# Kernel optimization log

Measured on AMD Instinct MI355X. Metric: run time of the kernel, lower is better.

Reference implementation:

```python
import jax, jax.numpy as jnp
import numpy as np
from jax import lax

NUM_LAYERS = 4
EPS_BN = 1e-5
EPS_AGG = 1e-6


def _bn(x, gamma, beta):
    # training-mode batch norm over the leading (node/edge) dim
    m = x.mean(axis=0)
    v = x.var(axis=0)
    return gamma * (x - m) / jnp.sqrt(v + EPS_BN) + beta


def setup_inputs() -> dict:
    key = jax.random.key(0)
    ks = jax.random.split(key, 32)
    N, E, D, L, K = 50000, 400000, 64, 128, 16
    s = 0.05
    inp = {
        'reads': jax.random.uniform(ks[0], (N, 4, L), jnp.float32),
        'src': jax.random.randint(ks[1], (E,), 0, N, jnp.int32),
        'dst': jax.random.randint(ks[2], (E,), 0, N, jnp.int32),
        'overlap_similarity': jax.random.uniform(ks[3], (E,), jnp.float32),
        'overlap_length': jax.random.normal(ks[4], (E,), jnp.float32),
        # sequence encoder conv: Conv1d(4 -> D, kernel K)
        'conv_w': jax.random.normal(ks[5], (D, 4, K), jnp.float32) * s,
        'conv_b': jnp.zeros((D,), jnp.float32),
        # edge encoder: Linear(2 -> D)
        'We': jax.random.normal(ks[6], (2, D), jnp.float32) * s,
        'be': jnp.zeros((D,), jnp.float32),
        # GatedGCN per-layer weights, stacked on leading layer dim
        'A1': jax.random.normal(ks[7], (NUM_LAYERS, D, D), jnp.float32) * s,
        'A2': jax.random.normal(ks[8], (NUM_LAYERS, D, D), jnp.float32) * s,
        'A3': jax.random.normal(ks[9], (NUM_LAYERS, D, D), jnp.float32) * s,
        'bA1': jnp.zeros((NUM_LAYERS, D), jnp.float32),
        'bA2': jnp.zeros((NUM_LAYERS, D), jnp.float32),
        'bA3': jnp.zeros((NUM_LAYERS, D), jnp.float32),
        'U': jax.random.normal(ks[10], (NUM_LAYERS, D, D), jnp.float32) * s,
        'V': jax.random.normal(ks[11], (NUM_LAYERS, D, D), jnp.float32) * s,
        'bU': jnp.zeros((NUM_LAYERS, D), jnp.float32),
        'bV': jnp.zeros((NUM_LAYERS, D), jnp.float32),
        'bn_h_gamma': jnp.ones((NUM_LAYERS, D), jnp.float32),
        'bn_h_beta': jnp.zeros((NUM_LAYERS, D), jnp.float32),
        'bn_e_gamma': jnp.ones((NUM_LAYERS, D), jnp.float32),
        'bn_e_beta': jnp.zeros((NUM_LAYERS, D), jnp.float32),
        # edge decoder MLP: Linear(3D -> D) -> ReLU -> Linear(D -> 1)
        'W1': jax.random.normal(ks[12], (3 * D, D), jnp.float32) * s,
        'b1': jnp.zeros((D,), jnp.float32),
        'W2': jax.random.normal(ks[13], (D, 1), jnp.float32) * s,
        'b2': jnp.zeros((1,), jnp.float32),
    }
    return inp


def reference(reads, src, dst, overlap_similarity, overlap_length,
              conv_w, conv_b, We, be,
              A1, A2, A3, bA1, bA2, bA3, U, V, bU, bV,
              bn_h_gamma, bn_h_beta, bn_e_gamma, bn_e_beta,
              W1, b1, W2, b2):
    N = reads.shape[0]
    # --- SequenceEncoder: Conv1d over one-hot reads, global max-pool ---
    hseq = lax.conv_general_dilated(
        reads, conv_w, window_strides=(1,), padding='VALID',
        dimension_numbers=('NCH', 'OIH', 'NCH'))  # [N, D, L-K+1]
    h = (hseq + conv_b[None, :, None]).max(axis=2)  # [N, D]
    # --- EdgeEncoder: Linear on [similarity, length] ---
    e = jnp.stack([overlap_similarity, overlap_length], axis=1) @ We + be  # [E, D]
    # --- stacked GatedGCN layers (gather src/dst, scatter-aggregate to dst) ---
    for l in range(NUM_LAYERS):
        hs = h[src]  # [E, D] gather
        hd = h[dst]
        e_hat = (hs @ A1[l] + bA1[l]) + (hd @ A2[l] + bA2[l]) + (e @ A3[l] + bA3[l])
        sigma = jax.nn.sigmoid(e_hat)  # edge gates
        Vh = hs @ V[l] + bV[l]
        num = jax.ops.segment_sum(sigma * Vh, dst, num_segments=N)  # [N, D]
        den = jax.ops.segment_sum(sigma, dst, num_segments=N)
        h_hat = (h @ U[l] + bU[l]) + num / (den + EPS_AGG)
        h = h + jax.nn.relu(_bn(h_hat, bn_h_gamma[l], bn_h_beta[l]))
        e = e + jax.nn.relu(_bn(e_hat, bn_e_gamma[l], bn_e_beta[l]))
    # --- EdgeDecoder: MLP on [h_src, h_dst, e] ---
    z = jnp.concatenate([h[src], h[dst], e], axis=1)  # [E, 3D]
    p = jax.nn.relu(z @ W1 + b1) @ W2 + b2  # [E, 1]
    return p
```

## Files before the change

kernel.cpp:

```cpp
#include <hip/hip_runtime.h>
#include <hip/hip_bf16.h>
#include <cstdint>
#include <cstddef>

#define DD 64

typedef __attribute__((ext_vector_type(8))) short short8;
typedef __attribute__((ext_vector_type(4))) float f32x4;

__device__ __forceinline__ float4 f4_0() { return make_float4(0.f, 0.f, 0.f, 0.f); }

__device__ __forceinline__ unsigned short f2bf(float f) {
  __hip_bfloat16 h = __float2bfloat16(f);
  return *reinterpret_cast<unsigned short*>(&h);
}
__device__ __forceinline__ float bfl(unsigned u) { return __uint_as_float(u << 16); }
__device__ __forceinline__ float bfh(unsigned u) { return __uint_as_float(u & 0xffff0000u); }
__device__ __forceinline__ float b2f(unsigned short u) {
  return __uint_as_float(((unsigned)u) << 16);
}

__device__ __forceinline__ short8 pack_bf16x8(float4 a, float4 b) {
  union { unsigned short us[8]; short8 v; } pk;
  pk.us[0] = f2bf(a.x); pk.us[1] = f2bf(a.y); pk.us[2] = f2bf(a.z); pk.us[3] = f2bf(a.w);
  pk.us[4] = f2bf(b.x); pk.us[5] = f2bf(b.y); pk.us[6] = f2bf(b.z); pk.us[7] = f2bf(b.w);
  return pk.v;
}

__device__ __forceinline__ short8 lds_frag(const unsigned short* p) {
  uint2 lo = *reinterpret_cast<const uint2*>(p);
  uint2 hi = *reinterpret_cast<const uint2*>(p + 4);
  union { unsigned u[4]; short8 v; } t;
  t.u[0] = lo.x; t.u[1] = lo.y; t.u[2] = hi.x; t.u[3] = hi.y;
  return t.v;
}
__device__ __forceinline__ short8 g_frag(const unsigned short* p) {
  return *reinterpret_cast<const short8*>(p);
}

__global__ __launch_bounds__(256) void k_hist(const int* __restrict__ dst,
                                              int* __restrict__ cnt, int E) {
  int j = blockIdx.x * 256 + threadIdx.x;
  if (j < E) atomicAdd(&cnt[dst[j]], 1);
}

__global__ __launch_bounds__(1024) void k_scan(const int* __restrict__ cnt,
                                               int* __restrict__ row_ptr,
                                               int* __restrict__ nxt, int N, int E) {
  __shared__ int wsum[16];
  __shared__ int carry_s;
  const int tid = threadIdx.x;
  const int wid = tid >> 6, lane = tid & 63;
  if (tid == 0) carry_s = 0;
  __syncthreads();
  const int ntl = (N + 4095) / 4096;
  for (int b = 0; b < ntl; ++b) {
    const int i0 = b * 4096 + tid * 4;
    int v0 = 0, v1 = 0, v2 = 0, v3 = 0;
    if (i0 + 3 < N) {
      int4 q = *reinterpret_cast<const int4*>(cnt + i0);
      v0 = q.x; v1 = q.y; v2 = q.z; v3 = q.w;
    } else {
      if (i0 < N) v0 = cnt[i0];
      if (i0 + 1 < N) v1 = cnt[i0 + 1];
      if (i0 + 2 < N) v2 = cnt[i0 + 2];
      if (i0 + 3 < N) v3 = cnt[i0 + 3];
    }
    const int tsum = v0 + v1 + v2 + v3;
    int x = tsum;
#pragma unroll
    for (int off = 1; off < 64; off <<= 1) {
      int y = __shfl_up(x, off, 64);
      if (lane >= off) x += y;
    }
    if (lane == 63) wsum[wid] = x;
    __syncthreads();
    if (wid == 0 && lane < 16) {
      int wv = wsum[lane];
#pragma unroll
      for (int off = 1; off < 16; off <<= 1) {
        int y = __shfl_up(wv, off, 64);
        if (lane >= off) wv += y;
      }
      wsum[lane] = wv;
    }
    __syncthreads();
    int base = carry_s + (wid > 0 ? wsum[wid - 1] : 0) + (x - tsum);
    int e1 = base + v0, e2 = e1 + v1, e3 = e2 + v2;
    if (i0 < N) { row_ptr[i0] = base; nxt[i0] = base; }
    if (i0 + 1 < N) { row_ptr[i0 + 1] = e1; nxt[i0 + 1] = e1; }
    if (i0 + 2 < N) { row_ptr[i0 + 2] = e2; nxt[i0 + 2] = e2; }
    if (i0 + 3 < N) { row_ptr[i0 + 3] = e3; nxt[i0 + 3] = e3; }
    __syncthreads();
    if (tid == 0) carry_s += wsum[15];
    __syncthreads();
  }
  if (tid == 0) row_ptr[N] = E;
}

__global__ __launch_bounds__(256) void k_scatter(const int* __restrict__ dst,
                                                 const int* __restrict__ src,
                                                 int* __restrict__ nxt,
                                                 int* __restrict__ order,
                                                 int* __restrict__ psrc,
                                                 int* __restrict__ pdst, int E) {
  int j = blockIdx.x * 256 + threadIdx.x;
  if (j >= E) return;
  int d = dst[j];
  int pos = atomicAdd(&nxt[d], 1);
  order[pos] = j;
  psrc[pos] = src[j];
  pdst[pos] = d;
}

__global__ __launch_bounds__(256) void k_prep(const float* __restrict__ A1,
                                              const float* __restrict__ A2,
                                              const float* __restrict__ V,
                                              const float* __restrict__ U,
                                              const float* __restrict__ A3,
                                              const float* __restrict__ W1,
                                              unsigned short* __restrict__ T) {
  const int b = blockIdx.x;
  const int tid = threadIdx.x;
  if (b < 20) {
    const int l = b / 5, m = b % 5;
    const float* srcp =
        (m == 0 ? A1 : m == 1 ? A2 : m == 2 ? V : m == 3 ? U : A3) + l * 4096;
    unsigned short* dstp = T + b * 4096;
    for (int i = tid; i < 4096; i += 256) {
      int n = i >> 6, k = i & 63;
      dstp[i] = f2bf(srcp[k * 64 + n]);
    }
  } else {
    unsigned short* dstp = T + 20 * 4096;
    for (int i = tid; i < 12288; i += 256) {
      int n = i / 192, k = i % 192;
      dstp[i] = f2bf(W1[k * 64 + n]);
    }
  }
}

__global__ __launch_bounds__(256) void k_conv_mfma(const float* __restrict__ reads,
                                                   const float* __restrict__ w,
                                                   const float* __restrict__ bias,
                                                   float* __restrict__ h, int N) {
  __shared__ unsigned short cp[4 * 4 * 4 * 144];
  const int tid = threadIdx.x;
  const int nb = blockIdx.x * 4;
  for (int task = tid; task < 576; task += 256) {
    const int node = task / 144;
    const int rem = task % 144;
    const int c = rem / 36;
    const int u = rem % 36;
    const int gn = nb + node;
    float4 v0 = f4_0(), v1 = f4_0();
    if (gn < N) {
      const float* rp = reads + (size_t)gn * 512 + c * 128 + 4 * u;
      if (u <= 31) v0 = *reinterpret_cast<const float4*>(rp);
      if (u <= 30) v1 = *reinterpret_cast<const float4*>(rp + 4);
    }
    unsigned pk0, pk1, pk2, pk3;
    asm("v_cvt_pk_bf16_f32 %0, %1, %2" : "=v"(pk0) : "v"(v0.x), "v"(v0.y));
    asm("v_cvt_pk_bf16_f32 %0, %1, %2" : "=v"(pk1) : "v"(v0.z), "v"(v0.w));
    asm("v_cvt_pk_bf16_f32 %0, %1, %2" : "=v"(pk2) : "v"(v1.x), "v"(v1.y));
    asm("v_cvt_pk_bf16_f32 %0, %1, %2" : "=v"(pk3) : "v"(v1.z), "v"(v1.w));
    const unsigned a0 = __builtin_amdgcn_alignbit(pk1, pk0, 16);
    const unsigned a1 = __builtin_amdgcn_alignbit(pk2, pk1, 16);
    const unsigned a2 = __builtin_amdgcn_alignbit(pk3, pk2, 16);
    const int base = ((node * 4 + c) * 4) * 144 + 4 * u;
    *reinterpret_cast<uint2*>(&cp[base + 0 * 144]) = make_uint2(pk0, pk1);
    *reinterpret_cast<uint2*>(&cp[base + 1 * 144]) = make_uint2(a0, a1);
    *reinterpret_cast<uint2*>(&cp[base + 2 * 144]) = make_uint2(pk1, pk2);
    *reinterpret_cast<uint2*>(&cp[base + 3 * 144]) = make_uint2(a1, a2);
  }
  __syncthreads();
  const int wid = tid >> 6, lane = tid & 63;
  const int gn = nb + wid;
  if (gn >= N) return;
  const int col = lane & 15, grp = lane >> 4;
  short8 wf[4][2];
#pragma unroll
  for (int nt = 0; nt < 4; ++nt)
#pragma unroll
    for (int ks = 0; ks < 2; ++ks) {
      const int d = nt * 16 + col;
      const int kb = ks * 32 + grp * 8;
      const float* wp = w + d * 64 + kb;
      float4 w0 = *reinterpret_cast<const float4*>(wp);
      float4 w1 = *reinterpret_cast<const float4*>(wp + 4);
      wf[nt][ks] = pack_bf16x8(w0, w1);
    }
  float vmax[4];
#pragma unroll
  for (int nt = 0; nt < 4; ++nt) vmax[nt] = -3.0e38f;
  const int s = col & 3;
  for (int mt = 0; mt < 8; ++mt) {
    const int t = mt * 16 + col;
    short8 af[2];
#pragma unroll
    for (int ks = 0; ks < 2; ++ks) {
      const int kbase = ks * 32 + grp * 8;
      const int c = kbase >> 4;
      const int kk0 = kbase & 15;
      const int q = (t - s) + kk0;
      af[ks] = lds_frag(&cp[((wid * 4 + c) * 4 + s) * 144 + q]);
    }
    f32x4 acc[4] = {};
#pragma unroll
    for (int ks = 0; ks < 2; ++ks)
#pragma unroll
      for (int nt = 0; nt < 4; ++nt)
        acc[nt] = __builtin_amdgcn_mfma_f32_16x16x32_bf16(af[ks], wf[nt][ks], acc[nt], 0, 0, 0);
    if (mt < 7) {
#pragma unroll
      for (int nt = 0; nt < 4; ++nt)
#pragma unroll
        for (int r = 0; r < 4; ++r) vmax[nt] = fmaxf(vmax[nt], acc[nt][r]);
    } else {
      if (grp == 0) {
#pragma unroll
        for (int nt = 0; nt < 4; ++nt) vmax[nt] = fmaxf(vmax[nt], acc[nt][0]);
      }
    }
  }
#pragma unroll
  for (int off = 16; off <= 32; off <<= 1)
#pragma unroll
    for (int nt = 0; nt < 4; ++nt)
      vmax[nt] = fmaxf(vmax[nt], __shfl_xor(vmax[nt], off, 64));
  if (grp == 0) {
#pragma unroll
    for (int nt = 0; nt < 4; ++nt) {
      const int d = nt * 16 + col;
      h[(size_t)gn * 64 + d] = vmax[nt] + bias[d];
    }
  }
}

__global__ __launch_bounds__(256) void k_node_mfma(const float* __restrict__ h_in,
                                                   float* __restrict__ h_out,
                                                   const float* __restrict__ hhat,
                                                   const float* __restrict__ sums_prev,
                                                   const float* __restrict__ gam,
                                                   const float* __restrict__ bet,
                                                   const unsigned short* __restrict__ Wt4,
                                                   const float* __restrict__ bA1,
                                                   const float* __restrict__ bA2,
                                                   const float* __restrict__ bV,
                                                   const float* __restrict__ bU,
                                                   unsigned short* __restrict__ XA1,
                                                   unsigned short* __restrict__ XA2,
                                                   unsigned short* __restrict__ XV,
                                                   float* __restrict__ XU,
                                                   int N, int hasupd) {
  __shared__ float s_coef[128];
  const int tid = threadIdx.x;
  if (hasupd) {
    if (tid < 64) {
      const float invR = 1.f / (float)N;
      float mean = sums_prev[tid] * invR;
      float var = sums_prev[64 + tid] * invR - mean * mean;
      float sc = gam[tid] * rsqrtf(var + 1e-5f);
      s_coef[tid] = sc;
      s_coef[64 + tid] = bet[tid] - mean * sc;
    }
    __syncthreads();
  }
  const int wid = tid >> 6, lane = tid & 63;
  const int col = lane & 15, g = lane >> 4;
  const int ntiles = (N + 15) / 16;
  for (int tw = blockIdx.x * 4 + wid; tw < ntiles; tw += gridDim.x * 4) {
    int n = tw * 16 + col;
    const bool valid = n < N;
    if (!valid) n = N - 1;
    short8 bfr[2];
#pragma unroll
    for (int ks = 0; ks < 2; ++ks) {
      const int c0 = ks * 32 + g * 8;
      const float* hp = h_in + (size_t)n * 64 + c0;
      float4 x0 = *reinterpret_cast<const float4*>(hp);
      float4 x1 = *reinterpret_cast<const float4*>(hp + 4);
      if (hasupd) {
        const float* yp = hhat + (size_t)n * 64 + c0;
        float4 y0 = *reinterpret_cast<const float4*>(yp);
        float4 y1 = *reinterpret_cast<const float4*>(yp + 4);
        float4 sc0 = *reinterpret_cast<const float4*>(&s_coef[c0]);
        float4 sc1 = *reinterpret_cast<const float4*>(&s_coef[c0 + 4]);
        float4 sh0 = *reinterpret_cast<const float4*>(&s_coef[64 + c0]);
        float4 sh1 = *reinterpret_cast<const float4*>(&s_coef[64 + c0 + 4]);
        x0.x += fmaxf(fmaf(sc0.x, y0.x, sh0.x), 0.f);
        x0.y += fmaxf(fmaf(sc0.y, y0.y, sh0.y), 0.f);
        x0.z += fmaxf(fmaf(sc0.z, y0.z, sh0.z), 0.f);
        x0.w += fmaxf(fmaf(sc0.w, y0.w, sh0.w), 0.f);
        x1.x += fmaxf(fmaf(sc1.x, y1.x, sh1.x), 0.f);
        x1.y += fmaxf(fmaf(sc1.y, y1.y, sh1.y), 0.f);
        x1.z += fmaxf(fmaf(sc1.z, y1.z, sh1.z), 0.f);
        x1.w += fmaxf(fmaf(sc1.w, y1.w, sh1.w), 0.f);
        if (valid) {
          float* op = h_out + (size_t)n * 64 + c0;
          *reinterpret_cast<float4*>(op) = x0;
          *reinterpret_cast<float4*>(op + 4) = x1;
        }
      }
      bfr[ks] = pack_bf16x8(x0, x1);
    }
#pragma unroll
    for (int m = 0; m < 4; ++m) {
      const unsigned short* Wm = Wt4 + m * 4096;
      f32x4 acc[4] = {};
#pragma unroll
      for (int ks = 0; ks < 2; ++ks) {
        const int ko = ks * 32 + g * 8;
#pragma unroll
        for (int mt = 0; mt < 4; ++mt) {
          short8 aa = g_frag(Wm + (mt * 16 + col) * 64 + ko);
          acc[mt] = __builtin_amdgcn_mfma_f32_16x16x32_bf16(aa, bfr[ks], acc[mt], 0, 0, 0);
        }
      }
      if (!valid) continue;
      const float* bb = (m == 0) ? bA1 : (m == 1) ? bA2 : (m == 2) ? bV : bU;
#pragma unroll
      for (int mt = 0; mt < 4; ++mt) {
        const int chb = mt * 16 + g * 4;
        float4 bv = *reinterpret_cast<const float4*>(bb + chb);
        float o0 = acc[mt][0] + bv.x;
        float o1 = acc[mt][1] + bv.y;
        float o2 = acc[mt][2] + bv.z;
        float o3 = acc[mt][3] + bv.w;
        if (m < 3) {
          unsigned short* X = (m == 0) ? XA1 : (m == 1) ? XA2 : XV;
          ushort4 ov;
          ov.x = f2bf(o0); ov.y = f2bf(o1); ov.z = f2bf(o2); ov.w = f2bf(o3);
          *reinterpret_cast<ushort4*>(X + (size_t)n * 64 + chb) = ov;
        } else {
          *reinterpret_cast<float4*>(XU + (size_t)n * 64 + chb) =
              make_float4(o0, o1, o2, o3);
        }
      }
    }
  }
}

__global__ __launch_bounds__(256) void k_edge_mfma0(unsigned short* __restrict__ e,
                                                    unsigned short* __restrict__ ehat_out,
                                                    const float* __restrict__ sim,
                                                    const float* __restrict__ olen,
                                                    const int* __restrict__ order,
                                                    const float* __restrict__ We,
                                                    const float* __restrict__ be,
                                                    const int* __restrict__ psrc,
                                                    const int* __restrict__ pdst,
                                                    const unsigned short* __restrict__ XA1,
                                                    const unsigned short* __restrict__ XA2,
                                                    const unsigned short* __restrict__ A3t,
                                                    const float* __restrict__ bA3,
                                                    float* __restrict__ sums_out, int E) {
  __shared__ float s_sums[128];
  const int tid = threadIdx.x;
  if (tid < 128) s_sums[tid] = 0.f;
  __syncthreads();
  const int wid = tid >> 6, lane = tid & 63;
  const int col = lane & 15, g = lane >> 4;
  short8 aa[4][2];
#pragma unroll
  for (int mt = 0; mt < 4; ++mt)
#pragma unroll
    for (int ks = 0; ks < 2; ++ks)
      aa[mt][ks] = g_frag(A3t + (mt * 16 + col) * 64 + ks * 32 + g * 8);
  float4 ba[4];
#pragma unroll
  for (int mt = 0; mt < 4; ++mt)
    ba[mt] = *reinterpret_cast<const float4*>(bA3 + mt * 16 + g * 4);
  float4 w0[2][2], w1[2][2], bev[2][2];
#pragma unroll
  for (int ks = 0; ks < 2; ++ks) {
    const int c0 = ks * 32 + g * 8;
    w0[ks][0] = *reinterpret_cast<const float4*>(We + c0);
    w0[ks][1] = *reinterpret_cast<const float4*>(We + c0 + 4);
    w1[ks][0] = *reinterpret_cast<const float4*>(We + 64 + c0);
    w1[ks][1] = *reinterpret_cast<const float4*>(We + 64 + c0 + 4);
    bev[ks][0] = *reinterpret_cast<const float4*>(be + c0);
    bev[ks][1] = *reinterpret_cast<const float4*>(be + c0 + 4);
  }
  float statS[16], statQ[16];
#pragma unroll
  for (int i = 0; i < 16; ++i) { statS[i] = 0.f; statQ[i] = 0.f; }
  const int ntiles = (E + 15) / 16;
  for (int tw = blockIdx.x * 4 + wid; tw < ntiles; tw += gridDim.x * 4) {
    int p = tw * 16 + col;
    const bool valid = p < E;
    if (!valid) p = E - 1;
    const int se = psrc[p], de = pdst[p];
    const int oe = order[p];
    const float sv = sim[oe], lv = olen[oe];
    short8 bfr[2];
#pragma unroll
    for (int ks = 0; ks < 2; ++ks) {
      float4 e0, e1;
      e0.x = fmaf(sv, w0[ks][0].x, fmaf(lv, w1[ks][0].x, bev[ks][0].x));
      e0.y = fmaf(sv, w0[ks][0].y, fmaf(lv, w1[ks][0].y, bev[ks][0].y));
      e0.z = fmaf(sv, w0[ks][0].z, fmaf(lv, w1[ks][0].z, bev[ks][0].z));
      e0.w = fmaf(sv, w0[ks][0].w, fmaf(lv, w1[ks][0].w, bev[ks][0].w));
      e1.x = fmaf(sv, w0[ks][1].x, fmaf(lv, w1[ks][1].x, bev[ks][1].x));
      e1.y = fmaf(sv, w0[ks][1].y, fmaf(lv, w1[ks][1].y, bev[ks][1].y));
      e1.z = fmaf(sv, w0[ks][1].z, fmaf(lv, w1[ks][1].z, bev[ks][1].z));
      e1.w = fmaf(sv, w0[ks][1].w, fmaf(lv, w1[ks][1].w, bev[ks][1].w));
      bfr[ks] = pack_bf16x8(e0, e1);
      if (valid)
        *reinterpret_cast<short8*>(e + (size_t)p * 64 + ks * 32 + g * 8) = bfr[ks];
    }
    f32x4 acc[4] = {};
#pragma unroll
    for (int ks = 0; ks < 2; ++ks)
#pragma unroll
      for (int mt = 0; mt < 4; ++mt)
        acc[mt] = __builtin_amdgcn_mfma_f32_16x16x32_bf16(aa[mt][ks], bfr[ks], acc[mt], 0, 0, 0);
    if (valid) {
#pragma unroll
      for (int mt = 0; mt < 4; ++mt) {
        const int chb = mt * 16 + g * 4;
        ushort4 x1 = *reinterpret_cast<const ushort4*>(XA1 + (size_t)se * 64 + chb);
        ushort4 x2 = *reinterpret_cast<const ushort4*>(XA2 + (size_t)de * 64 + chb);
        float o0 = acc[mt][0] + b2f(x1.x) + b2f(x2.x) + ba[mt].x;
        float o1 = acc[mt][1] + b2f(x1.y) + b2f(x2.y) + ba[mt].y;
        float o2 = acc[mt][2] + b2f(x1.z) + b2f(x2.z) + ba[mt].z;
        float o3 = acc[mt][3] + b2f(x1.w) + b2f(x2.w) + ba[mt].w;
        ushort4 ov;
        ov.x = f2bf(o0); ov.y = f2bf(o1); ov.z = f2bf(o2); ov.w = f2bf(o3);
        *reinterpret_cast<ushort4*>(ehat_out + (size_t)p * 64 + chb) = ov;
        statS[mt * 4 + 0] += o0; statQ[mt * 4 + 0] = fmaf(o0, o0, statQ[mt * 4 + 0]);
        statS[mt * 4 + 1] += o1; statQ[mt * 4 + 1] = fmaf(o1, o1, statQ[mt * 4 + 1]);
        statS[mt * 4 + 2] += o2; statQ[mt * 4 + 2] = fmaf(o2, o2, statQ[mt * 4 + 2]);
        statS[mt * 4 + 3] += o3; statQ[mt * 4 + 3] = fmaf(o3, o3, statQ[mt * 4 + 3]);
      }
    }
  }
#pragma unroll
  for (int off = 1; off <= 8; off <<= 1)
#pragma unroll
    for (int i = 0; i < 16; ++i) {
      statS[i] += __shfl_xor(statS[i], off, 64);
      statQ[i] += __shfl_xor(statQ[i], off, 64);
    }
  if (col == 0) {
#pragma unroll
    for (int mt = 0; mt < 4; ++mt)
#pragma unroll
      for (int c = 0; c < 4; ++c) {
        const int ch = mt * 16 + g * 4 + c;
        atomicAdd(&s_sums[ch], statS[mt * 4 + c]);
        atomicAdd(&s_sums[64 + ch], statQ[mt * 4 + c]);
      }
  }
  __syncthreads();
  if (tid < 128) atomicAdd(&sums_out[tid], s_sums[tid]);
}

__global__ __launch_bounds__(256) void k_edge_mfma(unsigned short* __restrict__ e,
                                                   const unsigned short* __restrict__ ehat_prev,
                                                   unsigned short* __restrict__ ehat_out,
                                                   const float* __restrict__ sums_prev,
                                                   const float* __restrict__ gprev,
                                                   const float* __restrict__ bprev,
                                                   const int* __restrict__ psrc,
                                                   const int* __restrict__ pdst,
                                                   const unsigned short* __restrict__ XA1,
                                                   const unsigned short* __restrict__ XA2,
                                                   const unsigned short* __restrict__ A3t,
                                                   const float* __restrict__ bA3,
                                                   float* __restrict__ sums_out, int E) {
  __shared__ float s_coef[128];
  __shared__ float s_sums[128];
  const int tid = threadIdx.x;
  if (tid < 128) s_sums[tid] = 0.f;
  if (tid < 64) {
    float mean = sums_prev[tid] / (float)E;
    float var = sums_prev[64 + tid] / (float)E - mean * mean;
    float sc = gprev[tid] * rsqrtf(var + 1e-5f);
    s_coef[tid] = sc;
    s_coef[64 + tid] = bprev[tid] - mean * sc;
  }
  __syncthreads();
  const int wid = tid >> 6, lane = tid & 63;
  const int col = lane & 15, g = lane >> 4;
  short8 aa[4][2];
#pragma unroll
  for (int mt = 0; mt < 4; ++mt)
#pragma unroll
    for (int ks = 0; ks < 2; ++ks)
      aa[mt][ks] = g_frag(A3t + (mt * 16 + col) * 64 + ks * 32 + g * 8);
  float4 ba[4];
#pragma unroll
  for (int mt = 0; mt < 4; ++mt)
    ba[mt] = *reinterpret_cast<const float4*>(bA3 + mt * 16 + g * 4);
  float statS[16], statQ[16];
#pragma unroll
  for (int i = 0; i < 16; ++i) { statS[i] = 0.f; statQ[i] = 0.f; }
  const int ntiles = (E + 15) / 16;
  for (int tw = blockIdx.x * 4 + wid; tw < ntiles; tw += gridDim.x * 4) {
    int p = tw * 16 + col;
    const bool valid = p < E;
    if (!valid) p = E - 1;
    const int se = psrc[p], de = pdst[p];
    short8 bfr[2];
#pragma unroll
    for (int ks = 0; ks < 2; ++ks) {
      const int c0 = ks * 32 + g * 8;
      uint4 eo = *reinterpret_cast<const uint4*>(e + (size_t)p * 64 + c0);
      float4 e0 = make_float4(bfl(eo.x), bfh(eo.x), bfl(eo.y), bfh(eo.y));
      float4 e1 = make_float4(bfl(eo.z), bfh(eo.z), bfl(eo.w), bfh(eo.w));
      uint4 hv = *reinterpret_cast<const uint4*>(ehat_prev + (size_t)p * 64 + c0);
      float4 sc0 = *reinterpret_cast<const float4*>(&s_coef[c0]);
      float4 sc1 = *reinterpret_cast<const float4*>(&s_coef[c0 + 4]);
      float4 sh0 = *reinterpret_cast<const float4*>(&s_coef[64 + c0]);
      float4 sh1 = *reinterpret_cast<const float4*>(&s_coef[64 + c0 + 4]);
      e0.x += fmaxf(fmaf(sc0.x, bfl(hv.x), sh0.x), 0.f);
      e0.y += fmaxf(fmaf(sc0.y, bfh(hv.x), sh0.y), 0.f);
      e0.z += fmaxf(fmaf(sc0.z, bfl(hv.y), sh0.z), 0.f);
      e0.w += fmaxf(fmaf(sc0.w, bfh(hv.y), sh0.w), 0.f);
      e1.x += fmaxf(fmaf(sc1.x, bfl(hv.z), sh1.x), 0.f);
      e1.y += fmaxf(fmaf(sc1.y, bfh(hv.z), sh1.y), 0.f);
      e1.z += fmaxf(fmaf(sc1.z, bfl(hv.w), sh1.z), 0.f);
      e1.w += fmaxf(fmaf(sc1.w, bfh(hv.w), sh1.w), 0.f);
      bfr[ks] = pack_bf16x8(e0, e1);
      if (valid)
        *reinterpret_cast<short8*>(e + (size_t)p * 64 + c0) = bfr[ks];
    }
    f32x4 acc[4] = {};
#pragma unroll
    for (int ks = 0; ks < 2; ++ks)
#pragma unroll
      for (int mt = 0; mt < 4; ++mt)
        acc[mt] = __builtin_amdgcn_mfma_f32_16x16x32_bf16(aa[mt][ks], bfr[ks], acc[mt], 0, 0, 0);
    if (valid) {
#pragma unroll
      for (int mt = 0; mt < 4; ++mt) {
        const int chb = mt * 16 + g * 4;
        ushort4 x1 = *reinterpret_cast<const ushort4*>(XA1 + (size_t)se * 64 + chb);
        ushort4 x2 = *reinterpret_cast<const ushort4*>(XA2 + (size_t)de * 64 + chb);
        float o0 = acc[mt][0] + b2f(x1.x) + b2f(x2.x) + ba[mt].x;
        float o1 = acc[mt][1] + b2f(x1.y) + b2f(x2.y) + ba[mt].y;
        float o2 = acc[mt][2] + b2f(x1.z) + b2f(x2.z) + ba[mt].z;
        float o3 = acc[mt][3] + b2f(x1.w) + b2f(x2.w) + ba[mt].w;
        ushort4 ov;
        ov.x = f2bf(o0); ov.y = f2bf(o1); ov.z = f2bf(o2); ov.w = f2bf(o3);
        *reinterpret_cast<ushort4*>(ehat_out + (size_t)p * 64 + chb) = ov;
        statS[mt * 4 + 0] += o0; statQ[mt * 4 + 0] = fmaf(o0, o0, statQ[mt * 4 + 0]);
        statS[mt * 4 + 1] += o1; statQ[mt * 4 + 1] = fmaf(o1, o1, statQ[mt * 4 + 1]);
        statS[mt * 4 + 2] += o2; statQ[mt * 4 + 2] = fmaf(o2, o2, statQ[mt * 4 + 2]);
        statS[mt * 4 + 3] += o3; statQ[mt * 4 + 3] = fmaf(o3, o3, statQ[mt * 4 + 3]);
      }
    }
  }
#pragma unroll
  for (int off = 1; off <= 8; off <<= 1)
#pragma unroll
    for (int i = 0; i < 16; ++i) {
      statS[i] += __shfl_xor(statS[i], off, 64);
      statQ[i] += __shfl_xor(statQ[i], off, 64);
    }
  if (col == 0) {
#pragma unroll
    for (int mt = 0; mt < 4; ++mt)
#pragma unroll
      for (int c = 0; c < 4; ++c) {
        const int ch = mt * 16 + g * 4 + c;
        atomicAdd(&s_sums[ch], statS[mt * 4 + c]);
        atomicAdd(&s_sums[64 + ch], statQ[mt * 4 + c]);
      }
  }
  __syncthreads();
  if (tid < 128) atomicAdd(&sums_out[tid], s_sums[tid]);
}

__global__ __launch_bounds__(256) void k_agg(const int* __restrict__ row_ptr,
                                             const int* __restrict__ psrc,
                                             const unsigned short* __restrict__ ehat,
                                             const unsigned short* __restrict__ XV,
                                             const float* __restrict__ XU,
                                             float* __restrict__ hhat,
                                             float* __restrict__ sums_h, int N) {
  __shared__ float s_sums[128];
  const int tid = threadIdx.x;
  if (tid < 128) s_sums[tid] = 0.f;
  __syncthreads();
  float sS[4] = {0.f, 0.f, 0.f, 0.f}, sQ[4] = {0.f, 0.f, 0.f, 0.f};
  const int total = N * 16;
  for (int idx = blockIdx.x * 256 + tid; idx < total; idx += gridDim.x * 256) {
    int n = idx >> 4, dc = (idx & 15) << 2;
    int beg = row_ptr[n], end = row_ptr[n + 1];
    float4 nm = f4_0(), dn = f4_0();
    for (int i = beg; i < end; ++i) {
      int sj = psrc[i];
      uint2 ev = *reinterpret_cast<const uint2*>(ehat + (size_t)i * 64 + dc);
      uint2 vv = *reinterpret_cast<const uint2*>(XV + (size_t)sj * 64 + dc);
      float s0 = 1.f / (1.f + __expf(-bfl(ev.x)));
      float s1 = 1.f / (1.f + __expf(-bfh(ev.x)));
      float s2 = 1.f / (1.f + __expf(-bfl(ev.y)));
      float s3 = 1.f / (1.f + __expf(-bfh(ev.y)));
      dn.x += s0; dn.y += s1; dn.z += s2; dn.w += s3;
      nm.x = fmaf(s0, bfl(vv.x), nm.x);
      nm.y = fmaf(s1, bfh(vv.x), nm.y);
      nm.z = fmaf(s2, bfl(vv.y), nm.z);
      nm.w = fmaf(s3, bfh(vv.y), nm.w);
    }
    float4 xu = *reinterpret_cast<const float4*>(XU + (size_t)n * 64 + dc);
    float h0 = xu.x + nm.x / (dn.x + 1e-6f);
    float h1 = xu.y + nm.y / (dn.y + 1e-6f);
    float h2 = xu.z + nm.z / (dn.z + 1e-6f);
    float h3 = xu.w + nm.w / (dn.w + 1e-6f);
    *reinterpret_cast<float4*>(hhat + (size_t)n * 64 + dc) = make_float4(h0, h1, h2, h3);
    sS[0] += h0; sQ[0] = fmaf(h0, h0, sQ[0]);
    sS[1] += h1; sQ[1] = fmaf(h1, h1, sQ[1]);
    sS[2] += h2; sQ[2] = fmaf(h2, h2, sQ[2]);
    sS[3] += h3; sQ[3] = fmaf(h3, h3, sQ[3]);
  }
#pragma unroll
  for (int off = 16; off <= 32; off <<= 1)
#pragma unroll
    for (int c = 0; c < 4; ++c) {
      sS[c] += __shfl_xor(sS[c], off, 64);
      sQ[c] += __shfl_xor(sQ[c], off, 64);
    }
  const int lane = tid & 63;
  if (lane < 16) {
    const int dc = lane << 2;
#pragma unroll
    for (int c = 0; c < 4; ++c) {
      atomicAdd(&s_sums[dc + c], sS[c]);
      atomicAdd(&s_sums[64 + dc + c], sQ[c]);
    }
  }
  __syncthreads();
  if (tid < 128) atomicAdd(&sums_h[tid], s_sums[tid]);
}

__global__ __launch_bounds__(256) void k_update_h(float* __restrict__ h,
                                                  const float* __restrict__ hhat,
                                                  const float* __restrict__ sums,
                                                  const float* __restrict__ gamma,
                                                  const float* __restrict__ beta, int R) {
  int idx = blockIdx.x * 256 + threadIdx.x;
  if (idx >= R * 16) return;
  int r = idx >> 4, dc = (idx & 15) << 2;
  const float invR = 1.f / (float)R;
  float4 sv = *reinterpret_cast<const float4*>(sums + dc);
  float4 qv = *reinterpret_cast<const float4*>(sums + 64 + dc);
  float4 gm = *reinterpret_cast<const float4*>(gamma + dc);
  float4 bt = *reinterpret_cast<const float4*>(beta + dc);
  float m0 = sv.x * invR, m1 = sv.y * invR, m2 = sv.z * invR, m3 = sv.w * invR;
  float c0 = gm.x * rsqrtf(qv.x * invR - m0 * m0 + 1e-5f);
  float c1 = gm.y * rsqrtf(qv.y * invR - m1 * m1 + 1e-5f);
  float c2 = gm.z * rsqrtf(qv.z * invR - m2 * m2 + 1e-5f);
  float c3 = gm.w * rsqrtf(qv.w * invR - m3 * m3 + 1e-5f);
  float h0 = bt.x - m0 * c0, h1 = bt.y - m1 * c1, h2 = bt.z - m2 * c2, h3 = bt.w - m3 * c3;
  size_t off = (size_t)r * 64 + dc;
  float4 y = *reinterpret_cast<const float4*>(hhat + off);
  float4 x = *reinterpret_cast<const float4*>(h + off);
  x.x += fmaxf(fmaf(c0, y.x, h0), 0.f);
  x.y += fmaxf(fmaf(c1, y.y, h1), 0.f);
  x.z += fmaxf(fmaf(c2, y.z, h2), 0.f);
  x.w += fmaxf(fmaf(c3, y.w, h3), 0.f);
  *reinterpret_cast<float4*>(h + off) = x;
}

__global__ __launch_bounds__(256) void k_decoder_mfma(const float* __restrict__ h,
                                                      const unsigned short* __restrict__ e,
                                                      const unsigned short* __restrict__ ehat3,
                                                      const float* __restrict__ sums_e3,
                                                      const float* __restrict__ ge3,
                                                      const float* __restrict__ be3,
                                                      const int* __restrict__ psrc,
                                                      const int* __restrict__ pdst,
                                                      const int* __restrict__ order,
                                                      const unsigned short* __restrict__ W1t,
                                                      const float* __restrict__ b1,
                                                      const float* __restrict__ W2,
                                                      const float* __restrict__ b2,
                                                      float* __restrict__ out, int E) {
  __shared__ unsigned short Wt[64 * 200];
  __shared__ float s_coef[128];
  const int tid = threadIdx.x;
  if (tid < 64) {
    float mean = sums_e3[tid] / (float)E;
    float var = sums_e3[64 + tid] / (float)E - mean * mean;
    float sc = ge3[tid] * rsqrtf(var + 1e-5f);
    s_coef[tid] = sc;
    s_coef[64 + tid] = be3[tid] - mean * sc;
  }
  for (int i = tid; i < 1536; i += 256) {
    int n = i / 24, kc = (i % 24) * 8;
    *reinterpret_cast<uint4*>(&Wt[n * 200 + kc]) =
        *reinterpret_cast<const uint4*>(W1t + n * 192 + kc);
  }
  __syncthreads();
  const int wid = tid >> 6, lane = tid & 63;
  const int col = lane & 15, g = lane >> 4;
  float b1v[4], w2v[4];
#pragma unroll
  for (int nt = 0; nt < 4; ++nt) { b1v[nt] = b1[nt * 16 + col]; w2v[nt] = W2[nt * 16 + col]; }
  const float bb2 = b2[0];
  const int ntiles = (E + 15) / 16;
  for (int tw = blockIdx.x * 4 + wid; tw < ntiles; tw += gridDim.x * 4) {
    const int eb = tw * 16;
    int p = eb + col;
    if (p >= E) p = E - 1;
    const int se = psrc[p], de = pdst[p];
    f32x4 acc[4] = {};
#pragma unroll
    for (int ks = 0; ks < 6; ++ks) {
      float4 a0, a1;
      if (ks < 4) {
        const float* ap = (ks < 2 ? h + (size_t)se * 64 : h + (size_t)de * 64) + (ks & 1) * 32 + g * 8;
        a0 = *reinterpret_cast<const float4*>(ap);
        a1 = *reinterpret_cast<const float4*>(ap + 4);
      } else {
        const int c0 = (ks - 4) * 32 + g * 8;
        uint4 eo = *reinterpret_cast<const uint4*>(e + (size_t)p * 64 + c0);
        a0 = make_float4(bfl(eo.x), bfh(eo.x), bfl(eo.y), bfh(eo.y));
        a1 = make_float4(bfl(eo.z), bfh(eo.z), bfl(eo.w), bfh(eo.w));
        uint4 hv = *reinterpret_cast<const uint4*>(ehat3 + (size_t)p * 64 + c0);
        float4 sc0 = *reinterpret_cast<const float4*>(&s_coef[c0]);
        float4 sc1 = *reinterpret_cast<const float4*>(&s_coef[c0 + 4]);
        float4 sh0 = *reinterpret_cast<const float4*>(&s_coef[64 + c0]);
        float4 sh1 = *reinterpret_cast<const float4*>(&s_coef[64 + c0 + 4]);
        a0.x += fmaxf(fmaf(sc0.x, bfl(hv.x), sh0.x), 0.f);
        a0.y += fmaxf(fmaf(sc0.y, bfh(hv.x), sh0.y), 0.f);
        a0.z += fmaxf(fmaf(sc0.z, bfl(hv.y), sh0.z), 0.f);
        a0.w += fmaxf(fmaf(sc0.w, bfh(hv.y), sh0.w), 0.f);
        a1.x += fmaxf(fmaf(sc1.x, bfl(hv.z), sh1.x), 0.f);
        a1.y += fmaxf(fmaf(sc1.y, bfh(hv.z), sh1.y), 0.f);
        a1.z += fmaxf(fmaf(sc1.z, bfl(hv.w), sh1.z), 0.f);
        a1.w += fmaxf(fmaf(sc1.w, bfh(hv.w), sh1.w), 0.f);
      }
      short8 af = pack_bf16x8(a0, a1);
#pragma unroll
      for (int nt = 0; nt < 4; ++nt) {
        short8 bb = lds_frag(&Wt[(nt * 16 + col) * 200 + ks * 32 + g * 8]);
        acc[nt] = __builtin_amdgcn_mfma_f32_16x16x32_bf16(af, bb, acc[nt], 0, 0, 0);
      }
    }
    float pr[4];
#pragma unroll
    for (int r = 0; r < 4; ++r) {
      float s = 0.f;
#pragma unroll
      for (int nt = 0; nt < 4; ++nt)
        s = fmaf(fmaxf(acc[nt][r] + b1v[nt], 0.f), w2v[nt], s);
      pr[r] = s;
    }
#pragma unroll
    for (int off = 1; off <= 8; off <<= 1)
#pragma unroll
      for (int r = 0; r < 4; ++r)
        pr[r] += __shfl_xor(pr[r], off, 64);
    if (col == 0) {
#pragma unroll
      for (int r = 0; r < 4; ++r) {
        int m = eb + g * 4 + r;
        if (m < E) out[order[m]] = pr[r] + bb2;
      }
    }
  }
}

extern "C" void kernel_launch(void* const* d_in, const int* in_sizes, int n_in,
                              void* d_out, int out_size, void* d_ws, size_t ws_size,
                              hipStream_t stream) {
  const float* reads  = (const float*)d_in[0];
  const int*   src    = (const int*)d_in[1];
  const int*   dst    = (const int*)d_in[2];
  const float* sim    = (const float*)d_in[3];
  const float* olen   = (const float*)d_in[4];
  const float* conv_w = (const float*)d_in[5];
  const float* conv_b = (const float*)d_in[6];
  const float* We     = (const float*)d_in[7];
  const float* be     = (const float*)d_in[8];
  const float* A1     = (const float*)d_in[9];
  const float* A2     = (const float*)d_in[10];
  const float* A3     = (const float*)d_in[11];
  const float* bA1    = (const float*)d_in[12];
  const float* bA2    = (const float*)d_in[13];
  const float* bA3    = (const float*)d_in[14];
  const float* U      = (const float*)d_in[15];
  const float* V      = (const float*)d_in[16];
  const float* bU     = (const float*)d_in[17];
  const float* bV     = (const float*)d_in[18];
  const float* bnhg   = (const float*)d_in[19];
  const float* bnhb   = (const float*)d_in[20];
  const float* bneg   = (const float*)d_in[21];
  const float* bneb   = (const float*)d_in[22];
  const float* W1     = (const float*)d_in[23];
  const float* b1     = (const float*)d_in[24];
  const float* W2     = (const float*)d_in[25];
  const float* b2     = (const float*)d_in[26];

  const int N = in_sizes[0] / 512;
  const int E = in_sizes[1];

  float* fp = (float*)d_ws;
  float* hA   = fp; fp += (size_t)N * 64;
  float* hB   = fp; fp += (size_t)N * 64;
  float* hhat = fp; fp += (size_t)N * 64;
  float* XU   = fp; fp += (size_t)N * 64;
  float* sums = fp; fp += 1024;
  unsigned short* up = (unsigned short*)fp;
  unsigned short* e     = up; up += (size_t)E * 64;
  unsigned short* ehatA = up; up += (size_t)E * 64;
  unsigned short* ehatB = up; up += (size_t)E * 64;
  unsigned short* XA1 = up; up += (size_t)N * 64;
  unsigned short* XA2 = up; up += (size_t)N * 64;
  unsigned short* XV  = up; up += (size_t)N * 64;
  unsigned short* Wt  = up; up += 20 * 4096 + 12288;
  int* ip = (int*)up;
  int* order   = ip; ip += E;
  int* psrc    = ip; ip += E;
  int* pdst    = ip; ip += E;
  int* cnt     = ip; ip += N;
  int* nxt     = ip; ip += N;
  int* row_ptr = ip; ip += N + 1;
  float* out = (float*)d_out;

  hipMemsetAsync(cnt, 0, sizeof(int) * N, stream);
  hipMemsetAsync(sums, 0, sizeof(float) * 1024, stream);
  k_hist<<<(E + 255) / 256, 256, 0, stream>>>(dst, cnt, E);
  k_prep<<<21, 256, 0, stream>>>(A1, A2, V, U, A3, W1, Wt);
  k_scan<<<1, 1024, 0, stream>>>(cnt, row_ptr, nxt, N, E);
  k_scatter<<<(E + 255) / 256, 256, 0, stream>>>(dst, src, nxt, order, psrc, pdst, E);

  k_conv_mfma<<<(N + 3) / 4, 256, 0, stream>>>(reads, conv_w, conv_b, hA, N);

  const int PBLK = 1024;
  const int NPB = 512;
  float* hin = hA;
  float* hout = hB;
  unsigned short* ehat_cur = ehatA;
  unsigned short* ehat_prev = ehatB;
  for (int l = 0; l < 4; ++l) {
    ehat_cur = (l & 1) ? ehatB : ehatA;
    ehat_prev = (l & 1) ? ehatA : ehatB;
    float* sums_e = sums + l * 128;
    float* sums_h = sums + 512 + l * 128;
    k_node_mfma<<<NPB, 256, 0, stream>>>(
        hin, (l > 0) ? hout : nullptr, hhat,
        (l > 0) ? (sums + 512 + (l - 1) * 128) : sums,
        bnhg + (l > 0 ? (l - 1) * 64 : 0), bnhb + (l > 0 ? (l - 1) * 64 : 0),
        Wt + l * 5 * 4096,
        bA1 + l * 64, bA2 + l * 64, bV + l * 64, bU + l * 64,
        XA1, XA2, XV, XU, N, l > 0 ? 1 : 0);
    if (l > 0) { float* t = hin; hin = hout; hout = t; }
    if (l == 0) {
      k_edge_mfma0<<<PBLK, 256, 0, stream>>>(
          e, ehat_cur, sim, olen, order, We, be, psrc, pdst, XA1, XA2,
          Wt + 4 * 4096, bA3, sums_e, E);
    } else {
      k_edge_mfma<<<PBLK, 256, 0, stream>>>(
          e, ehat_prev, ehat_cur, sums + (l - 1) * 128,
          bneg + (l - 1) * 64, bneb + (l - 1) * 64,
          psrc, pdst, XA1, XA2, Wt + (l * 5 + 4) * 4096, bA3 + l * 64, sums_e, E);
    }
    k_agg<<<PBLK, 256, 0, stream>>>(row_ptr, psrc, ehat_cur, XV, XU, hhat, sums_h, N);
  }

  k_update_h<<<(N * 16 + 255) / 256, 256, 0, stream>>>(
      hin, hhat, sums + 512 + 3 * 128, bnhg + 3 * 64, bnhb + 3 * 64, N);
  k_decoder_mfma<<<PBLK, 256, 0, stream>>>(
      hin, e, ehat_cur, sums + 3 * 128, bneg + 3 * 64, bneb + 3 * 64,
      psrc, pdst, order, Wt + 20 * 4096, b1, W2, b2, out, E);
}
```

Measured before the change: 865.1 us.

## Make conv kernel persistent with double-buffered LDS prefetch; enlarge edge grids

The conv encoder now runs as a persistent grid of at most 1024 blocks that loop over 4-node groups. Each block loads the next group's reads into registers while computing the current group from a double-buffered LDS tile, and converts the bf16 weight fragments only once per block. The edge and decoder kernels also move from 1024 to 2048 blocks. The costs are extra registers for the prefetch and less occupancy-based latency hiding in the conv kernel. It relies on a single __syncthreads per iteration being enough to order the LDS buffer reuse.

```diff
diff --git a/kernel.cpp b/kernel.cpp
--- a/kernel.cpp
+++ b/kernel.cpp
@@ -140,44 +140,63 @@
   }
 }
 
+struct ConvRegs { float4 v[3][2]; };
+
+__device__ __forceinline__ void conv_load(const float* __restrict__ reads, int N,
+                                          int g, int tid, ConvRegs& R) {
+#pragma unroll
+  for (int it = 0; it < 3; ++it) {
+    const int task = tid + it * 256;
+    R.v[it][0] = f4_0(); R.v[it][1] = f4_0();
+    if (task < 576) {
+      const int node = task / 144, rem = task % 144;
+      const int c = rem / 36, u = rem % 36;
+      const int gn = g * 4 + node;
+      if (gn < N) {
+        const float* rp = reads + (size_t)gn * 512 + c * 128 + 4 * u;
+        if (u <= 31) R.v[it][0] = *reinterpret_cast<const float4*>(rp);
+        if (u <= 30) R.v[it][1] = *reinterpret_cast<const float4*>(rp + 4);
+      }
+    }
+  }
+}
+
+__device__ __forceinline__ void conv_write(unsigned short* __restrict__ cbuf,
+                                           int tid, const ConvRegs& R) {
+#pragma unroll
+  for (int it = 0; it < 3; ++it) {
+    const int task = tid + it * 256;
+    if (task < 576) {
+      const int node = task / 144, rem = task % 144;
+      const int c = rem / 36, u = rem % 36;
+      const float4 v0 = R.v[it][0], v1 = R.v[it][1];
+      unsigned pk0, pk1, pk2, pk3;
+      asm("v_cvt_pk_bf16_f32 %0, %1, %2" : "=v"(pk0) : "v"(v0.x), "v"(v0.y));
+      asm("v_cvt_pk_bf16_f32 %0, %1, %2" : "=v"(pk1) : "v"(v0.z), "v"(v0.w));
+      asm("v_cvt_pk_bf16_f32 %0, %1, %2" : "=v"(pk2) : "v"(v1.x), "v"(v1.y));
+      asm("v_cvt_pk_bf16_f32 %0, %1, %2" : "=v"(pk3) : "v"(v1.z), "v"(v1.w));
+      const unsigned a0 = __builtin_amdgcn_alignbit(pk1, pk0, 16);
+      const unsigned a1 = __builtin_amdgcn_alignbit(pk2, pk1, 16);
+      const unsigned a2 = __builtin_amdgcn_alignbit(pk3, pk2, 16);
+      const int base = ((node * 4 + c) * 4) * 144 + 4 * u;
+      *reinterpret_cast<uint2*>(&cbuf[base + 0 * 144]) = make_uint2(pk0, pk1);
+      *reinterpret_cast<uint2*>(&cbuf[base + 1 * 144]) = make_uint2(a0, a1);
+      *reinterpret_cast<uint2*>(&cbuf[base + 2 * 144]) = make_uint2(pk1, pk2);
+      *reinterpret_cast<uint2*>(&cbuf[base + 3 * 144]) = make_uint2(a1, a2);
+    }
+  }
+}
+
 __global__ __launch_bounds__(256) void k_conv_mfma(const float* __restrict__ reads,
                                                    const float* __restrict__ w,
                                                    const float* __restrict__ bias,
                                                    float* __restrict__ h, int N) {
-  __shared__ unsigned short cp[4 * 4 * 4 * 144];
+  __shared__ unsigned short cp[2][4 * 4 * 4 * 144];
   const int tid = threadIdx.x;
-  const int nb = blockIdx.x * 4;
-  for (int task = tid; task < 576; task += 256) {
-    const int node = task / 144;
-    const int rem = task % 144;
-    const int c = rem / 36;
-    const int u = rem % 36;
-    const int gn = nb + node;
-    float4 v0 = f4_0(), v1 = f4_0();
-    if (gn < N) {
-      const float* rp = reads + (size_t)gn * 512 + c * 128 + 4 * u;
-      if (u <= 31) v0 = *reinterpret_cast<const float4*>(rp);
-      if (u <= 30) v1 = *reinterpret_cast<const float4*>(rp + 4);
-    }
-    unsigned pk0, pk1, pk2, pk3;
-    asm("v_cvt_pk_bf16_f32 %0, %1, %2" : "=v"(pk0) : "v"(v0.x), "v"(v0.y));
-    asm("v_cvt_pk_bf16_f32 %0, %1, %2" : "=v"(pk1) : "v"(v0.z), "v"(v0.w));
-    asm("v_cvt_pk_bf16_f32 %0, %1, %2" : "=v"(pk2) : "v"(v1.x), "v"(v1.y));
-    asm("v_cvt_pk_bf16_f32 %0, %1, %2" : "=v"(pk3) : "v"(v1.z), "v"(v1.w));
-    const unsigned a0 = __builtin_amdgcn_alignbit(pk1, pk0, 16);
-    const unsigned a1 = __builtin_amdgcn_alignbit(pk2, pk1, 16);
-    const unsigned a2 = __builtin_amdgcn_alignbit(pk3, pk2, 16);
-    const int base = ((node * 4 + c) * 4) * 144 + 4 * u;
-    *reinterpret_cast<uint2*>(&cp[base + 0 * 144]) = make_uint2(pk0, pk1);
-    *reinterpret_cast<uint2*>(&cp[base + 1 * 144]) = make_uint2(a0, a1);
-    *reinterpret_cast<uint2*>(&cp[base + 2 * 144]) = make_uint2(pk1, pk2);
-    *reinterpret_cast<uint2*>(&cp[base + 3 * 144]) = make_uint2(a1, a2);
-  }
-  __syncthreads();
   const int wid = tid >> 6, lane = tid & 63;
-  const int gn = nb + wid;
-  if (gn >= N) return;
   const int col = lane & 15, grp = lane >> 4;
+  const int ngroups = (N + 3) / 4;
+  if ((int)blockIdx.x >= ngroups) return;
   short8 wf[4][2];
 #pragma unroll
   for (int nt = 0; nt < 4; ++nt)
@@ -190,50 +209,65 @@
       float4 w1 = *reinterpret_cast<const float4*>(wp + 4);
       wf[nt][ks] = pack_bf16x8(w0, w1);
     }
-  float vmax[4];
-#pragma unroll
-  for (int nt = 0; nt < 4; ++nt) vmax[nt] = -3.0e38f;
+  ConvRegs RA, RB;
+  conv_load(reads, N, blockIdx.x, tid, RA);
+  int p = 0;
   const int s = col & 3;
-  for (int mt = 0; mt < 8; ++mt) {
-    const int t = mt * 16 + col;
-    short8 af[2];
-#pragma unroll
-    for (int ks = 0; ks < 2; ++ks) {
-      const int kbase = ks * 32 + grp * 8;
-      const int c = kbase >> 4;
-      const int kk0 = kbase & 15;
-      const int q = (t - s) + kk0;
-      af[ks] = lds_frag(&cp[((wid * 4 + c) * 4 + s) * 144 + q]);
-    }
-    f32x4 acc[4] = {};
-#pragma unroll
-    for (int ks = 0; ks < 2; ++ks)
-#pragma unroll
-      for (int nt = 0; nt < 4; ++nt)
-        acc[nt] = __builtin_amdgcn_mfma_f32_16x16x32_bf16(af[ks], wf[nt][ks], acc[nt], 0, 0, 0);
-    if (mt < 7) {
-#pragma unroll
-      for (int nt = 0; nt < 4; ++nt)
-#pragma unroll
-        for (int r = 0; r < 4; ++r) vmax[nt] = fmaxf(vmax[nt], acc[nt][r]);
-    } else {
+  for (int g = blockIdx.x; g < ngroups; g += gridDim.x) {
+    conv_write(&cp[p][0], tid, RA);
+    const int gnext = g + gridDim.x;
+    if (gnext < ngroups) conv_load(reads, N, gnext, tid, RB);
+    __syncthreads();
+    const int gn = g * 4 + wid;
+    if (gn < N) {
+      const unsigned short* cbuf = &cp[p][0];
+      float vmax[4];
+#pragma unroll
+      for (int nt = 0; nt < 4; ++nt) vmax[nt] = -3.0e38f;
+      for (int mt = 0; mt < 8; ++mt) {
+        const int t = mt * 16 + col;
+        short8 af[2];
+#pragma unroll
+        for (int ks = 0; ks < 2; ++ks) {
+          const int kbase = ks * 32 + grp * 8;
+          const int c = kbase >> 4;
+          const int kk0 = kbase & 15;
+          const int q = (t - s) + kk0;
+          af[ks] = lds_frag(&cbuf[((wid * 4 + c) * 4 + s) * 144 + q]);
+        }
+        f32x4 acc[4] = {};
+#pragma unroll
+        for (int ks = 0; ks < 2; ++ks)
+#pragma unroll
+          for (int nt = 0; nt < 4; ++nt)
+            acc[nt] = __builtin_amdgcn_mfma_f32_16x16x32_bf16(af[ks], wf[nt][ks], acc[nt], 0, 0, 0);
+        if (mt < 7) {
+#pragma unroll
+          for (int nt = 0; nt < 4; ++nt)
+#pragma unroll
+            for (int r = 0; r < 4; ++r) vmax[nt] = fmaxf(vmax[nt], acc[nt][r]);
+        } else {
+          if (grp == 0) {
+#pragma unroll
+            for (int nt = 0; nt < 4; ++nt) vmax[nt] = fmaxf(vmax[nt], acc[nt][0]);
+          }
+        }
+      }
+#pragma unroll
+      for (int off = 16; off <= 32; off <<= 1)
+#pragma unroll
+        for (int nt = 0; nt < 4; ++nt)
+          vmax[nt] = fmaxf(vmax[nt], __shfl_xor(vmax[nt], off, 64));
       if (grp == 0) {
 #pragma unroll
-        for (int nt = 0; nt < 4; ++nt) vmax[nt] = fmaxf(vmax[nt], acc[nt][0]);
-      }
-    }
-  }
-#pragma unroll
-  for (int off = 16; off <= 32; off <<= 1)
-#pragma unroll
-    for (int nt = 0; nt < 4; ++nt)
-      vmax[nt] = fmaxf(vmax[nt], __shfl_xor(vmax[nt], off, 64));
-  if (grp == 0) {
-#pragma unroll
-    for (int nt = 0; nt < 4; ++nt) {
-      const int d = nt * 16 + col;
-      h[(size_t)gn * 64 + d] = vmax[nt] + bias[d];
-    }
+        for (int nt = 0; nt < 4; ++nt) {
+          const int d = nt * 16 + col;
+          h[(size_t)gn * 64 + d] = vmax[nt] + bias[d];
+        }
+      }
+    }
+    p ^= 1;
+    RA = RB;
   }
 }
 
@@ -828,9 +862,12 @@
   k_scan<<<1, 1024, 0, stream>>>(cnt, row_ptr, nxt, N, E);
   k_scatter<<<(E + 255) / 256, 256, 0, stream>>>(dst, src, nxt, order, psrc, pdst, E);
 
-  k_conv_mfma<<<(N + 3) / 4, 256, 0, stream>>>(reads, conv_w, conv_b, hA, N);
-
-  const int PBLK = 1024;
+  const int ngroups = (N + 3) / 4;
+  const int CG = ngroups < 1024 ? ngroups : 1024;
+  k_conv_mfma<<<CG, 256, 0, stream>>>(reads, conv_w, conv_b, hA, N);
+
+  const int EPBLK = 2048;
+  const int APBLK = 1024;
   const int NPB = 512;
   float* hin = hA;
   float* hout = hB;
@@ -850,21 +887,21 @@
         XA1, XA2, XV, XU, N, l > 0 ? 1 : 0);
     if (l > 0) { float* t = hin; hin = hout; hout = t; }
     if (l == 0) {
-      k_edge_mfma0<<<PBLK, 256, 0, stream>>>(
+      k_edge_mfma0<<<EPBLK, 256, 0, stream>>>(
           e, ehat_cur, sim, olen, order, We, be, psrc, pdst, XA1, XA2,
           Wt + 4 * 4096, bA3, sums_e, E);
     } else {
-      k_edge_mfma<<<PBLK, 256, 0, stream>>>(
+      k_edge_mfma<<<EPBLK, 256, 0, stream>>>(
           e, ehat_prev, ehat_cur, sums + (l - 1) * 128,
           bneg + (l - 1) * 64, bneb + (l - 1) * 64,
           psrc, pdst, XA1, XA2, Wt + (l * 5 + 4) * 4096, bA3 + l * 64, sums_e, E);
     }
-    k_agg<<<PBLK, 256, 0, stream>>>(row_ptr, psrc, ehat_cur, XV, XU, hhat, sums_h, N);
+    k_agg<<<APBLK, 256, 0, stream>>>(row_ptr, psrc, ehat_cur, XV, XU, hhat, sums_h, N);
   }
 
   k_update_h<<<(N * 16 + 255) / 256, 256, 0, stream>>>(
       hin, hhat, sums + 512 + 3 * 128, bnhg + 3 * 64, bnhb + 3 * 64, N);
-  k_decoder_mfma<<<PBLK, 256, 0, stream>>>(
+  k_decoder_mfma<<<EPBLK, 256, 0, stream>>>(
       hin, e, ehat_cur, sums + 3 * 128, bneg + 3 * 64, bneb + 3 * 64,
       psrc, pdst, order, Wt + 20 * 4096, b1, W2, b2, out, E);
 }
```

After: 856.0 us. About the same (-1.0%).
